# Kernel tuning notes

Measured on AMD Instinct MI355X. Metric: run time of the kernel, lower is better.

The kernel has to match this reference:

```python
import jax, jax.numpy as jnp
import numpy as np

B, L, D = 2, 2048, 1024
H, E = 16, 64  # n_heads, per-head dim (E_q=E_k=E_v)
EPS = 1e-5


def _layernorm(x):
    # fresh nn.LayerNorm each forward: gamma=1, beta=0, eps=1e-5 (biased var)
    mu = jnp.mean(x, axis=-1, keepdims=True)
    var = jnp.mean(jnp.square(x - mu), axis=-1, keepdims=True)
    return (x - mu) * jax.lax.rsqrt(var + EPS)


def setup_inputs() -> dict:
    key = jax.random.key(0)
    ks = jax.random.split(key, 9)
    s_in = 1.0 / np.sqrt(D)
    s_ctx = 1.0 / np.sqrt(H * E)
    return {
        "query": jax.random.normal(ks[0], (B, L, D), jnp.float32),
        "key": jax.random.normal(ks[1], (B, L, D), jnp.float32),
        "value": jax.random.normal(ks[2], (B, L, D), jnp.float32),
        # torch nn.Linear weights are [out_features, in_features]
        "W_Q": jax.random.uniform(ks[3], (H * E, D), jnp.float32, -s_in, s_in),
        "W_K": jax.random.uniform(ks[4], (H * E, D), jnp.float32, -s_in, s_in),
        "W_V": jax.random.uniform(ks[5], (H * E, D), jnp.float32, -s_in, s_in),
        "W_O": jax.random.uniform(ks[6], (D, H * E), jnp.float32, -s_ctx, s_ctx),
        "fc_w": jax.random.uniform(ks[7], (D, D), jnp.float32, -s_in, s_in),
        "fc_b": jax.random.uniform(ks[8], (D,), jnp.float32, -s_in, s_in),
    }


def reference(query, key, value, W_Q, W_K, W_V, W_O, fc_w, fc_b):
    b = query.shape[0]
    # projections -> [B, H, L, E]
    q = (query @ W_Q.T).reshape(b, -1, H, E).transpose(0, 2, 1, 3)
    k = (key @ W_K.T).reshape(b, -1, H, E).transpose(0, 2, 1, 3)
    v = (value @ W_V.T).reshape(b, -1, H, E).transpose(0, 2, 1, 3)
    scores = jnp.einsum('bhqe,bhke->bhqk', q, k) / np.sqrt(E).astype(np.float32)
    A = jax.nn.softmax(scores, axis=-1)                 # [B,H,Lq,Lk]
    ctx = jnp.einsum('bhqk,bhke->bhqe', A, v)           # [B,H,L,E]
    ctx = ctx.transpose(0, 2, 1, 3).reshape(b, -1, H * E)
    attn_out = ctx @ W_O.T                               # dropout = identity (eval)
    x = _layernorm(attn_out + query)
    out = x @ fc_w.T + fc_b                              # dropout = identity (eval)
    out = _layernorm(x + out)
    return out
```

## Files before the change

### kernel.cpp

```cpp
#include <hip/hip_runtime.h>
#include <stdint.h>

typedef unsigned short u16;
typedef __bf16 bf16x8 __attribute__((ext_vector_type(8)));
typedef __bf16 bf16x4 __attribute__((ext_vector_type(4)));
typedef short s16x4 __attribute__((ext_vector_type(4)));
typedef float f32x4 __attribute__((ext_vector_type(4)));

#define MFMA16(a,b,c) __builtin_amdgcn_mfma_f32_16x16x32_bf16((a),(b),(c),0,0,0)

__device__ __forceinline__ f32x4 mfma_k16(bf16x4 a, bf16x4 b, f32x4 c){
#if __has_builtin(__builtin_amdgcn_mfma_f32_16x16x16_bf16)
  return __builtin_amdgcn_mfma_f32_16x16x16_bf16(a, b, c, 0, 0, 0);
#elif __has_builtin(__builtin_amdgcn_mfma_f32_16x16x16bf16_1k)
  s16x4 ai, bi;
  __builtin_memcpy(&ai, &a, 8);
  __builtin_memcpy(&bi, &b, 8);
  return __builtin_amdgcn_mfma_f32_16x16x16bf16_1k(ai, bi, c, 0, 0, 0);
#else
  asm("v_mfma_f32_16x16x16_bf16 %0, %1, %2, %0" : "+v"(c) : "v"(a), "v"(b));
  return c;
#endif
}

__device__ __forceinline__ bf16x4 pack4(float a, float b, float c, float d){
  bf16x4 r; r[0]=(__bf16)a; r[1]=(__bf16)b; r[2]=(__bf16)c; r[3]=(__bf16)d; return r;
}

__device__ __forceinline__ void gl2lds16(const void* g, void* l){
  __builtin_amdgcn_global_load_lds(
      (const __attribute__((address_space(1))) unsigned int*)g,
      (__attribute__((address_space(3))) unsigned int*)l, 16, 0, 0);
}

__device__ __forceinline__ bf16x8 ldsfrag(const u16* base, int row, int gr){
  return *(const bf16x8*)(base + row * 64 + ((gr ^ (row & 7)) << 3));
}
__device__ __forceinline__ bf16x4 ldsfrag64(const u16* base, int row, int gr, int h){
  return *(const bf16x4*)(base + row * 64 + ((gr ^ (row & 7)) << 3) + (h << 2));
}

template<int NB, int BN>
__device__ __forceinline__ void gemm_core(const u16* __restrict__ A,
                                          const u16* __restrict__ Bt,
                                          int N, int K, int mode,
                                          void* __restrict__ Cout,
                                          const float* __restrict__ bias,
                                          float oscale)
{
  constexpr int NF = BN / 32;
  __shared__ u16 Al[NB][128 * 64];
  __shared__ u16 Bl[NB][BN * 64];
  const int tid  = threadIdx.x;
  const int lane = tid & 63;
  const int w    = tid >> 6;
  const int wr   = w >> 1, wc = w & 1;
  const int l15  = lane & 15, g = lane >> 4;
  const int rowBase = blockIdx.y << 7;
  const int colBase = blockIdx.x * BN;

  const int srow = tid >> 3;
  const int swz  = ((tid & 7) ^ (srow & 7)) << 3;
  const u16* Ag = A  + (size_t)(rowBase + srow) * K + swz;
  const u16* Bg = Bt + (size_t)(colBase + srow) * K + swz;

  f32x4 acc[4][NF];
#pragma unroll
  for (int m = 0; m < 4; ++m)
#pragma unroll
    for (int n = 0; n < NF; ++n) acc[m][n] = f32x4{0.f, 0.f, 0.f, 0.f};

  auto stage = [&](int buf, int k0) {
#pragma unroll
    for (int i = 0; i < 4; ++i)
      gl2lds16(Ag + (size_t)(i * 32) * K + k0, Al[buf] + i * 2048 + w * 512);
#pragma unroll
    for (int i = 0; i < BN / 32; ++i)
      gl2lds16(Bg + (size_t)(i * 32) * K + k0, Bl[buf] + i * 2048 + w * 512);
  };
  auto compute = [&](int buf) {
    __builtin_amdgcn_s_setprio(1);
#pragma unroll
    for (int kk = 0; kk < 2; ++kk) {
      bf16x8 af[4], bfr[NF];
#pragma unroll
      for (int m = 0; m < 4; ++m) af[m]  = ldsfrag(Al[buf], wr * 64 + m * 16 + l15, kk * 4 + g);
#pragma unroll
      for (int n = 0; n < NF; ++n) bfr[n] = ldsfrag(Bl[buf], wc * (BN/2) + n * 16 + l15, kk * 4 + g);
#pragma unroll
      for (int m = 0; m < 4; ++m)
#pragma unroll
        for (int n = 0; n < NF; ++n)
          acc[m][n] = MFMA16(af[m], bfr[n], acc[m][n]);
    }
    __builtin_amdgcn_s_setprio(0);
  };

  if (NB == 2) {
    stage(0, 0);
    __syncthreads();
    int cur = 0;
    for (int k0 = 0; k0 < K; k0 += 64) {
      if (k0 + 64 < K) stage(cur ^ 1, k0 + 64);
      compute(cur);
      __syncthreads();
      cur ^= 1;
    }
  } else {
    for (int k0 = 0; k0 < K; k0 += 64) {
      stage(0, k0);
      __syncthreads();
      compute(0);
      __syncthreads();
    }
  }

#pragma unroll
  for (int m = 0; m < 4; ++m) {
#pragma unroll
    for (int n = 0; n < NF; ++n) {
      const int row0 = rowBase + wr * 64 + m * 16 + g * 4;
      const int col  = colBase + wc * (BN/2) + n * 16 + l15;
      if (mode == 1) {
        const int b = row0 >> 11, l = row0 & 2047;
        const int h = col >> 6,  e = col & 63;
        *(bf16x4*)((u16*)Cout + ((size_t)((((b << 4) + h) << 6) | e) << 11) + l) =
            pack4(acc[m][n][0], acc[m][n][1], acc[m][n][2], acc[m][n][3]);
      } else {
        const float bb = (mode == 4) ? bias[col] : 0.f;
#pragma unroll
        for (int r = 0; r < 4; ++r) {
          const int row = row0 + r;
          const float v = acc[m][n][r];
          if (mode == 0) {
            *(__bf16*)((u16*)Cout + (size_t)row * N + col) = (__bf16)(v * oscale);
          } else {
            *(__bf16*)((u16*)Cout + (size_t)row * N + col) = (__bf16)(v + bb);
          }
        }
      }
    }
  }
}

#define QSCALE 0.18033688011112042f

__global__ __launch_bounds__(256) void k_proj(
    const u16* __restrict__ qb, const u16* __restrict__ kb, const u16* __restrict__ vb,
    const u16* __restrict__ wq, const u16* __restrict__ wk, const u16* __restrict__ wv,
    u16* __restrict__ Qp, u16* __restrict__ Kp, u16* __restrict__ Vt)
{
  const int z = blockIdx.z;
  const u16* A = (z == 0) ? qb : (z == 1) ? kb : vb;
  const u16* B = (z == 0) ? wq : (z == 1) ? wk : wv;
  void* C = (z == 0) ? (void*)Qp : (z == 1) ? (void*)Kp : (void*)Vt;
  gemm_core<2, 64>(A, B, 1024, 1024, (z == 2) ? 1 : 0, C, nullptr, (z == 0) ? QSCALE : 1.0f);
}

__global__ __launch_bounds__(256) void k_gemm_o(const u16* __restrict__ A,
                                                const u16* __restrict__ B,
                                                u16* __restrict__ C)
{ gemm_core<2, 64>(A, B, 1024, 1024, 0, (void*)C, nullptr, 1.0f); }

__global__ __launch_bounds__(256) void k_gemm_fc(const u16* __restrict__ A,
                                                 const u16* __restrict__ B,
                                                 u16* __restrict__ C,
                                                 const float* __restrict__ bias)
{ gemm_core<2, 64>(A, B, 1024, 1024, 4, (void*)C, bias, 1.0f); }

__global__ __launch_bounds__(256, 4) void k_attn(const u16* __restrict__ Qp,
                                                 const u16* __restrict__ Kp,
                                                 const u16* __restrict__ Vt,
                                                 float* __restrict__ Opart,
                                                 float* __restrict__ dpart)
{
  __shared__ u16 Klds[2][64 * 64];
  __shared__ u16 Vlds[2][64 * 64];

  const int tid = threadIdx.x, lane = tid & 63, w = tid >> 6;
  const int l15 = lane & 15, g = lane >> 4;
  const int bh = blockIdx.y, b = bh >> 4, h = bh & 15;
  const int q0 = blockIdx.x << 7;
  const int half = blockIdx.z;
  const int kvbase = half << 10;

  bf16x8 bq[2][2];
#pragma unroll
  for (int u = 0; u < 2; ++u) {
    const u16* Qr = Qp + (((size_t)((b << 11) + q0 + (w << 5) + (u << 4) + l15)) << 10)
                  + (h << 6) + (g << 3);
    bq[u][0] = *(const bf16x8*)(Qr);
    bq[u][1] = *(const bf16x8*)(Qr + 32);
  }

  const f32x4 zero4 = {0.f, 0.f, 0.f, 0.f};
  f32x4 o0[4], o1[4];
#pragma unroll
  for (int f = 0; f < 4; ++f) { o0[f] = zero4; o1[f] = zero4; }
  float ds0 = 0.f, ds1 = 0.f;

  const int srow = tid >> 3;
  const int swz  = ((tid & 7) ^ (srow & 7)) << 3;
  const u16* Kg = Kp + (((size_t)((b << 11) + kvbase + srow)) << 10) + (h << 6) + swz;
  const u16* Vg = Vt + (((size_t)((bh << 6) + srow)) << 11) + kvbase + swz;

  auto stage = [&](int buf, int j0) {
#pragma unroll
    for (int i = 0; i < 2; ++i) {
      gl2lds16(Kg + ((size_t)(j0 + i * 32) << 10), Klds[buf] + i * 2048 + w * 512);
      gl2lds16(Vg + ((size_t)(i * 32) << 11) + j0, Vlds[buf] + i * 2048 + w * 512);
    }
  };

  stage(0, 0);
  __syncthreads();
  int cur = 0;

  for (int j0 = 0; j0 < 1024; j0 += 64) {
    if (j0 + 64 < 1024) stage(cur ^ 1, j0 + 64);

    f32x4 s0[4], s1[4];
    __builtin_amdgcn_s_setprio(1);
#pragma unroll
    for (int f = 0; f < 4; ++f) {
      const bf16x8 ka = ldsfrag(Klds[cur], f * 16 + l15, g);
      const bf16x8 kb = ldsfrag(Klds[cur], f * 16 + l15, 4 + g);
      s0[f] = MFMA16(ka, bq[0][0], zero4);
      s0[f] = MFMA16(kb, bq[0][1], s0[f]);
      s1[f] = MFMA16(ka, bq[1][0], zero4);
      s1[f] = MFMA16(kb, bq[1][1], s1[f]);
    }
    __builtin_amdgcn_s_setprio(0);

    bf16x4 p0[4], p1[4];
#pragma unroll
    for (int f = 0; f < 4; ++f) {
      const float a0 = __builtin_amdgcn_exp2f(s0[f][0]);
      const float a1 = __builtin_amdgcn_exp2f(s0[f][1]);
      const float a2 = __builtin_amdgcn_exp2f(s0[f][2]);
      const float a3 = __builtin_amdgcn_exp2f(s0[f][3]);
      ds0 += (a0 + a1) + (a2 + a3);
      p0[f] = pack4(a0, a1, a2, a3);
      const float c0 = __builtin_amdgcn_exp2f(s1[f][0]);
      const float c1 = __builtin_amdgcn_exp2f(s1[f][1]);
      const float c2 = __builtin_amdgcn_exp2f(s1[f][2]);
      const float c3 = __builtin_amdgcn_exp2f(s1[f][3]);
      ds1 += (c0 + c1) + (c2 + c3);
      p1[f] = pack4(c0, c1, c2, c3);
    }

    __builtin_amdgcn_s_setprio(1);
#pragma unroll
    for (int fe = 0; fe < 4; ++fe) {
#pragma unroll
      for (int f = 0; f < 4; ++f) {
        const bf16x4 va = ldsfrag64(Vlds[cur], fe * 16 + l15, 2 * f + (g >> 1), g & 1);
        o0[fe] = mfma_k16(va, p0[f], o0[fe]);
        o1[fe] = mfma_k16(va, p1[f], o1[fe]);
      }
    }
    __builtin_amdgcn_s_setprio(0);
    __syncthreads();
    cur ^= 1;
  }

  ds0 += __shfl_xor(ds0, 16, 64);
  ds0 += __shfl_xor(ds0, 32, 64);
  ds1 += __shfl_xor(ds1, 16, 64);
  ds1 += __shfl_xor(ds1, 32, 64);

  const int brow0 = (b << 11) + q0 + (w << 5) + l15;
  const int brow1 = brow0 + 16;
  float* Op = Opart + ((size_t)half << 22);
#pragma unroll
  for (int f = 0; f < 4; ++f) {
    *(f32x4*)(Op + ((size_t)brow0 << 10) + (h << 6) + f * 16 + (g << 2)) = o0[f];
    *(f32x4*)(Op + ((size_t)brow1 << 10) + (h << 6) + f * 16 + (g << 2)) = o1[f];
  }
  if (g == 0) {
    dpart[(half << 16) + (brow0 << 4) + h] = ds0;
    dpart[(half << 16) + (brow1 << 4) + h] = ds1;
  }
}

__global__ __launch_bounds__(256) void k_combine(const float* __restrict__ Opart,
                                                 const float* __restrict__ dpart,
                                                 u16* __restrict__ ctx)
{
  const int row = blockIdx.x, tid = threadIdx.x;
  const int h = tid >> 4;
  const float d = dpart[(row << 4) + h] + dpart[(1 << 16) + (row << 4) + h];
  const float inv = 1.0f / d;
  const f32x4 p0 = ((const f32x4*)(Opart + ((size_t)row << 10)))[tid];
  const f32x4 p1 = ((const f32x4*)(Opart + (1u << 22) + ((size_t)row << 10)))[tid];
  ((bf16x4*)(ctx + ((size_t)row << 10)))[tid] =
      pack4((p0[0] + p1[0]) * inv, (p0[1] + p1[1]) * inv,
            (p0[2] + p1[2]) * inv, (p0[3] + p1[3]) * inv);
}

__device__ __forceinline__ void ln_stats(float4 t, int tid, float& mean, float& inv){
  float s = t.x + t.y + t.z + t.w;
  float q = t.x * t.x + t.y * t.y + t.z * t.z + t.w * t.w;
#pragma unroll
  for (int d = 1; d < 64; d <<= 1) {
    s += __shfl_xor(s, d, 64);
    q += __shfl_xor(q, d, 64);
  }
  __shared__ float ps[4], pq[4];
  const int w = tid >> 6;
  if ((tid & 63) == 0) { ps[w] = s; pq[w] = q; }
  __syncthreads();
  s = ps[0] + ps[1] + ps[2] + ps[3];
  q = pq[0] + pq[1] + pq[2] + pq[3];
  mean = s * (1.0f / 1024.0f);
  const float var = q * (1.0f / 1024.0f) - mean * mean;
  inv = rsqrtf(var + 1e-5f);
}

__global__ __launch_bounds__(256) void k_ln1(const u16* __restrict__ a,
                                             const float* __restrict__ res,
                                             u16* __restrict__ xb)
{
  const int row = blockIdx.x, tid = threadIdx.x;
  const size_t base = (size_t)row << 10;
  const bf16x4 av = ((const bf16x4*)(a + base))[tid];
  const float4 rr = ((const float4*)(res + base))[tid];
  float4 t;
  t.x = (float)av[0] + rr.x; t.y = (float)av[1] + rr.y;
  t.z = (float)av[2] + rr.z; t.w = (float)av[3] + rr.w;
  float mean, inv;
  ln_stats(t, tid, mean, inv);
  ((bf16x4*)(xb + base))[tid] = pack4((t.x - mean) * inv, (t.y - mean) * inv,
                                      (t.z - mean) * inv, (t.w - mean) * inv);
}

__global__ __launch_bounds__(256) void k_ln2(const u16* __restrict__ a,
                                             const u16* __restrict__ res,
                                             float* __restrict__ out)
{
  const int row = blockIdx.x, tid = threadIdx.x;
  const size_t base = (size_t)row << 10;
  const bf16x4 av = ((const bf16x4*)(a + base))[tid];
  const bf16x4 rv = ((const bf16x4*)(res + base))[tid];
  float4 t;
  t.x = (float)av[0] + (float)rv[0]; t.y = (float)av[1] + (float)rv[1];
  t.z = (float)av[2] + (float)rv[2]; t.w = (float)av[3] + (float)rv[3];
  float mean, inv;
  ln_stats(t, tid, mean, inv);
  float4 o;
  o.x = (t.x - mean) * inv; o.y = (t.y - mean) * inv;
  o.z = (t.z - mean) * inv; o.w = (t.w - mean) * inv;
  ((float4*)(out + base))[tid] = o;
}

__global__ __launch_bounds__(256) void k_cvt3(const float* __restrict__ q,
                                              const float* __restrict__ k,
                                              const float* __restrict__ v,
                                              u16* __restrict__ qo,
                                              u16* __restrict__ ko,
                                              u16* __restrict__ vo)
{
  const int z = blockIdx.y;
  const float* src = (z == 0) ? q : (z == 1) ? k : v;
  u16* dst = (z == 0) ? qo : (z == 1) ? ko : vo;
  const int i = blockIdx.x * 256 + threadIdx.x;
  const float4 t = ((const float4*)src)[i];
  ((bf16x4*)dst)[i] = pack4(t.x, t.y, t.z, t.w);
}

__global__ __launch_bounds__(256) void k_cvt5(const float* __restrict__ a0,
                                              const float* __restrict__ a1,
                                              const float* __restrict__ a2,
                                              const float* __restrict__ a3,
                                              const float* __restrict__ a4,
                                              u16* __restrict__ o0, u16* __restrict__ o1,
                                              u16* __restrict__ o2, u16* __restrict__ o3,
                                              u16* __restrict__ o4)
{
  const int z = blockIdx.y;
  const float* src = (z == 0) ? a0 : (z == 1) ? a1 : (z == 2) ? a2 : (z == 3) ? a3 : a4;
  u16* dst = (z == 0) ? o0 : (z == 1) ? o1 : (z == 2) ? o2 : (z == 3) ? o3 : o4;
  const int i = blockIdx.x * 256 + threadIdx.x;
  const float4 t = ((const float4*)src)[i];
  ((bf16x4*)dst)[i] = pack4(t.x, t.y, t.z, t.w);
}

extern "C" void kernel_launch(void* const* d_in, const int* in_sizes, int n_in,
                              void* d_out, int out_size, void* d_ws, size_t ws_size,
                              hipStream_t stream)
{
  (void)in_sizes; (void)n_in; (void)out_size; (void)ws_size;
  const float* query = (const float*)d_in[0];
  const float* key   = (const float*)d_in[1];
  const float* value = (const float*)d_in[2];
  const float* W_Q   = (const float*)d_in[3];
  const float* W_K   = (const float*)d_in[4];
  const float* W_V   = (const float*)d_in[5];
  const float* W_O   = (const float*)d_in[6];
  const float* fc_w  = (const float*)d_in[7];
  const float* fc_b  = (const float*)d_in[8];
  float* out = (float*)d_out;
  char* ws = (char*)d_ws;

  u16*   qb    = (u16*)(ws + 0);
  u16*   kb    = (u16*)(ws + 8388608);
  u16*   vb    = (u16*)(ws + 16777216);
  u16*   wq    = (u16*)(ws + 25165824);
  u16*   wk    = (u16*)(ws + 27262976);
  u16*   wv    = (u16*)(ws + 29360128);
  u16*   wo    = (u16*)(ws + 31457280);
  u16*   fw    = (u16*)(ws + 33554432);
  u16*   Qp    = (u16*)(ws + 35651584);
  u16*   Kp    = (u16*)(ws + 44040192);
  u16*   Vt    = (u16*)(ws + 52428800);
  u16*   ctx   = (u16*)(ws + 60817408);
  float* Opart = (float*)(ws + 69206016);
  float* dpart = (float*)(ws + 102760448);
  u16*   attnb = (u16*)(ws + 69206016);
  u16*   xb    = vb;
  u16*   yb    = qb;

  k_cvt3<<<dim3(4096, 3), 256, 0, stream>>>(query, key, value, qb, kb, vb);
  k_cvt5<<<dim3(1024, 5), 256, 0, stream>>>(W_Q, W_K, W_V, W_O, fc_w, wq, wk, wv, wo, fw);
  k_proj<<<dim3(16, 32, 3), 256, 0, stream>>>(qb, kb, vb, wq, wk, wv, Qp, Kp, Vt);
  k_attn<<<dim3(16, 32, 2), 256, 0, stream>>>(Qp, Kp, Vt, Opart, dpart);
  k_combine<<<dim3(4096), 256, 0, stream>>>(Opart, dpart, ctx);
  k_gemm_o<<<dim3(16, 32), 256, 0, stream>>>(ctx, wo, attnb);
  k_ln1<<<dim3(4096), 256, 0, stream>>>(attnb, query, xb);
  k_gemm_fc<<<dim3(16, 32), 256, 0, stream>>>(xb, fw, yb, fc_b);
  k_ln2<<<dim3(4096), 256, 0, stream>>>(yb, xb, out);
}
```

Measured before the change: 159.1 us.

## Fuse fp32-to-bf16 input conversion into projection GEMM and store attention partials as bf16

The projection GEMM now reads the fp32 query/key/value activations directly. It converts them to bf16 in registers and writes them into LDS, software-pipelined across the K loop, which removes the separate k_cvt3 kernel and its bf16 round-trip through memory. The split-KV attention partial outputs are also stored as bf16 instead of fp32, which halves the write and read traffic of the combine step. In exchange the A operand loses its async global-to-LDS path and needs extra registers, and rounding the unnormalized partials to bf16 adds a small amount of error.

```diff
diff --git a/kernel.cpp b/kernel.cpp
--- a/kernel.cpp
+++ b/kernel.cpp
@@ -26,6 +26,12 @@
 __device__ __forceinline__ bf16x4 pack4(float a, float b, float c, float d){
   bf16x4 r; r[0]=(__bf16)a; r[1]=(__bf16)b; r[2]=(__bf16)c; r[3]=(__bf16)d; return r;
 }
+__device__ __forceinline__ bf16x8 pack8(float4 a, float4 b){
+  bf16x8 r;
+  r[0]=(__bf16)a.x; r[1]=(__bf16)a.y; r[2]=(__bf16)a.z; r[3]=(__bf16)a.w;
+  r[4]=(__bf16)b.x; r[5]=(__bf16)b.y; r[6]=(__bf16)b.z; r[7]=(__bf16)b.w;
+  return r;
+}
 
 __device__ __forceinline__ void gl2lds16(const void* g, void* l){
   __builtin_amdgcn_global_load_lds(
@@ -40,8 +46,8 @@
   return *(const bf16x4*)(base + row * 64 + ((gr ^ (row & 7)) << 3) + (h << 2));
 }
 
-template<int NB, int BN>
-__device__ __forceinline__ void gemm_core(const u16* __restrict__ A,
+template<int BN, bool AF32>
+__device__ __forceinline__ void gemm_core(const void* __restrict__ Araw,
                                           const u16* __restrict__ Bt,
                                           int N, int K, int mode,
                                           void* __restrict__ Cout,
@@ -49,8 +55,8 @@
                                           float oscale)
 {
   constexpr int NF = BN / 32;
-  __shared__ u16 Al[NB][128 * 64];
-  __shared__ u16 Bl[NB][BN * 64];
+  __shared__ u16 Al[2][128 * 64];
+  __shared__ u16 Bl[2][BN * 64];
   const int tid  = threadIdx.x;
   const int lane = tid & 63;
   const int w    = tid >> 6;
@@ -61,8 +67,9 @@
 
   const int srow = tid >> 3;
   const int swz  = ((tid & 7) ^ (srow & 7)) << 3;
-  const u16* Ag = A  + (size_t)(rowBase + srow) * K + swz;
-  const u16* Bg = Bt + (size_t)(colBase + srow) * K + swz;
+  const u16*   Ag  = AF32 ? nullptr : (const u16*)Araw + (size_t)(rowBase + srow) * K + swz;
+  const float* Agf = AF32 ? (const float*)Araw + (size_t)(rowBase + srow) * K + swz : nullptr;
+  const u16*   Bg  = Bt + (size_t)(colBase + srow) * K + swz;
 
   f32x4 acc[4][NF];
 #pragma unroll
@@ -70,10 +77,28 @@
 #pragma unroll
     for (int n = 0; n < NF; ++n) acc[m][n] = f32x4{0.f, 0.f, 0.f, 0.f};
 
-  auto stage = [&](int buf, int k0) {
+  float4 ar[4][2];
+  auto loadA = [&](int k0) {
+    if (AF32) {
+#pragma unroll
+      for (int i = 0; i < 4; ++i) {
+        const float* p = Agf + (size_t)(i * 32) * K + k0;
+        ar[i][0] = *(const float4*)p;
+        ar[i][1] = *(const float4*)(p + 4);
+      }
+    }
+  };
+  auto writeA = [&](int buf) {
+#pragma unroll
+    for (int i = 0; i < 4; ++i)
+      *(bf16x8*)(Al[buf] + i * 2048 + tid * 8) = pack8(ar[i][0], ar[i][1]);
+  };
+  auto stageA = [&](int buf, int k0) {
 #pragma unroll
     for (int i = 0; i < 4; ++i)
       gl2lds16(Ag + (size_t)(i * 32) * K + k0, Al[buf] + i * 2048 + w * 512);
+  };
+  auto stageB = [&](int buf, int k0) {
 #pragma unroll
     for (int i = 0; i < BN / 32; ++i)
       gl2lds16(Bg + (size_t)(i * 32) * K + k0, Bl[buf] + i * 2048 + w * 512);
@@ -96,23 +121,21 @@
     __builtin_amdgcn_s_setprio(0);
   };
 
-  if (NB == 2) {
-    stage(0, 0);
+  if (AF32) { loadA(0); stageB(0, 0); writeA(0); }
+  else      { stageA(0, 0); stageB(0, 0); }
+  __syncthreads();
+  int cur = 0;
+  for (int k0 = 0; k0 < K; k0 += 64) {
+    const bool more = (k0 + 64) < K;
+    if (more) {
+      if (AF32) loadA(k0 + 64);
+      else      stageA(cur ^ 1, k0 + 64);
+      stageB(cur ^ 1, k0 + 64);
+    }
+    compute(cur);
+    if (more && AF32) writeA(cur ^ 1);
     __syncthreads();
-    int cur = 0;
-    for (int k0 = 0; k0 < K; k0 += 64) {
-      if (k0 + 64 < K) stage(cur ^ 1, k0 + 64);
-      compute(cur);
-      __syncthreads();
-      cur ^= 1;
-    }
-  } else {
-    for (int k0 = 0; k0 < K; k0 += 64) {
-      stage(0, k0);
-      __syncthreads();
-      compute(0);
-      __syncthreads();
-    }
+    cur ^= 1;
   }
 
 #pragma unroll
@@ -146,32 +169,32 @@
 #define QSCALE 0.18033688011112042f
 
 __global__ __launch_bounds__(256) void k_proj(
-    const u16* __restrict__ qb, const u16* __restrict__ kb, const u16* __restrict__ vb,
+    const float* __restrict__ qf, const float* __restrict__ kf, const float* __restrict__ vf,
     const u16* __restrict__ wq, const u16* __restrict__ wk, const u16* __restrict__ wv,
     u16* __restrict__ Qp, u16* __restrict__ Kp, u16* __restrict__ Vt)
 {
   const int z = blockIdx.z;
-  const u16* A = (z == 0) ? qb : (z == 1) ? kb : vb;
+  const float* A = (z == 0) ? qf : (z == 1) ? kf : vf;
   const u16* B = (z == 0) ? wq : (z == 1) ? wk : wv;
   void* C = (z == 0) ? (void*)Qp : (z == 1) ? (void*)Kp : (void*)Vt;
-  gemm_core<2, 64>(A, B, 1024, 1024, (z == 2) ? 1 : 0, C, nullptr, (z == 0) ? QSCALE : 1.0f);
+  gemm_core<64, true>(A, B, 1024, 1024, (z == 2) ? 1 : 0, C, nullptr, (z == 0) ? QSCALE : 1.0f);
 }
 
 __global__ __launch_bounds__(256) void k_gemm_o(const u16* __restrict__ A,
                                                 const u16* __restrict__ B,
                                                 u16* __restrict__ C)
-{ gemm_core<2, 64>(A, B, 1024, 1024, 0, (void*)C, nullptr, 1.0f); }
+{ gemm_core<64, false>(A, B, 1024, 1024, 0, (void*)C, nullptr, 1.0f); }
 
 __global__ __launch_bounds__(256) void k_gemm_fc(const u16* __restrict__ A,
                                                  const u16* __restrict__ B,
                                                  u16* __restrict__ C,
                                                  const float* __restrict__ bias)
-{ gemm_core<2, 64>(A, B, 1024, 1024, 4, (void*)C, bias, 1.0f); }
+{ gemm_core<64, false>(A, B, 1024, 1024, 4, (void*)C, bias, 1.0f); }
 
 __global__ __launch_bounds__(256, 4) void k_attn(const u16* __restrict__ Qp,
                                                  const u16* __restrict__ Kp,
                                                  const u16* __restrict__ Vt,
-                                                 float* __restrict__ Opart,
+                                                 u16* __restrict__ Opart,
                                                  float* __restrict__ dpart)
 {
   __shared__ u16 Klds[2][64 * 64];
@@ -271,11 +294,13 @@
 
   const int brow0 = (b << 11) + q0 + (w << 5) + l15;
   const int brow1 = brow0 + 16;
-  float* Op = Opart + ((size_t)half << 22);
+  u16* Op = Opart + ((size_t)half << 22);
 #pragma unroll
   for (int f = 0; f < 4; ++f) {
-    *(f32x4*)(Op + ((size_t)brow0 << 10) + (h << 6) + f * 16 + (g << 2)) = o0[f];
-    *(f32x4*)(Op + ((size_t)brow1 << 10) + (h << 6) + f * 16 + (g << 2)) = o1[f];
+    *(bf16x4*)(Op + (((size_t)brow0) << 10) + (h << 6) + f * 16 + (g << 2)) =
+        pack4(o0[f][0], o0[f][1], o0[f][2], o0[f][3]);
+    *(bf16x4*)(Op + (((size_t)brow1) << 10) + (h << 6) + f * 16 + (g << 2)) =
+        pack4(o1[f][0], o1[f][1], o1[f][2], o1[f][3]);
   }
   if (g == 0) {
     dpart[(half << 16) + (brow0 << 4) + h] = ds0;
@@ -283,7 +308,7 @@
   }
 }
 
-__global__ __launch_bounds__(256) void k_combine(const float* __restrict__ Opart,
+__global__ __launch_bounds__(256) void k_combine(const u16* __restrict__ Opart,
                                                  const float* __restrict__ dpart,
                                                  u16* __restrict__ ctx)
 {
@@ -291,11 +316,11 @@
   const int h = tid >> 4;
   const float d = dpart[(row << 4) + h] + dpart[(1 << 16) + (row << 4) + h];
   const float inv = 1.0f / d;
-  const f32x4 p0 = ((const f32x4*)(Opart + ((size_t)row << 10)))[tid];
-  const f32x4 p1 = ((const f32x4*)(Opart + (1u << 22) + ((size_t)row << 10)))[tid];
+  const bf16x4 p0 = ((const bf16x4*)(Opart + ((size_t)row << 10)))[tid];
+  const bf16x4 p1 = ((const bf16x4*)(Opart + (1u << 22) + ((size_t)row << 10)))[tid];
   ((bf16x4*)(ctx + ((size_t)row << 10)))[tid] =
-      pack4((p0[0] + p1[0]) * inv, (p0[1] + p1[1]) * inv,
-            (p0[2] + p1[2]) * inv, (p0[3] + p1[3]) * inv);
+      pack4(((float)p0[0] + (float)p1[0]) * inv, ((float)p0[1] + (float)p1[1]) * inv,
+            ((float)p0[2] + (float)p1[2]) * inv, ((float)p0[3] + (float)p1[3]) * inv);
 }
 
 __device__ __forceinline__ void ln_stats(float4 t, int tid, float& mean, float& inv){
@@ -353,21 +378,6 @@
   ((float4*)(out + base))[tid] = o;
 }
 
-__global__ __launch_bounds__(256) void k_cvt3(const float* __restrict__ q,
-                                              const float* __restrict__ k,
-                                              const float* __restrict__ v,
-                                              u16* __restrict__ qo,
-                                              u16* __restrict__ ko,
-                                              u16* __restrict__ vo)
-{
-  const int z = blockIdx.y;
-  const float* src = (z == 0) ? q : (z == 1) ? k : v;
-  u16* dst = (z == 0) ? qo : (z == 1) ? ko : vo;
-  const int i = blockIdx.x * 256 + threadIdx.x;
-  const float4 t = ((const float4*)src)[i];
-  ((bf16x4*)dst)[i] = pack4(t.x, t.y, t.z, t.w);
-}
-
 __global__ __launch_bounds__(256) void k_cvt5(const float* __restrict__ a0,
                                               const float* __restrict__ a1,
                                               const float* __restrict__ a2,
@@ -402,9 +412,8 @@
   float* out = (float*)d_out;
   char* ws = (char*)d_ws;
 
-  u16*   qb    = (u16*)(ws + 0);
-  u16*   kb    = (u16*)(ws + 8388608);
-  u16*   vb    = (u16*)(ws + 16777216);
+  u16*   xb    = (u16*)(ws + 0);
+  u16*   yb    = (u16*)(ws + 8388608);
   u16*   wq    = (u16*)(ws + 25165824);
   u16*   wk    = (u16*)(ws + 27262976);
   u16*   wv    = (u16*)(ws + 29360128);
@@ -414,15 +423,12 @@
   u16*   Kp    = (u16*)(ws + 44040192);
   u16*   Vt    = (u16*)(ws + 52428800);
   u16*   ctx   = (u16*)(ws + 60817408);
-  float* Opart = (float*)(ws + 69206016);
-  float* dpart = (float*)(ws + 102760448);
+  u16*   Opart = (u16*)(ws + 69206016);
+  float* dpart = (float*)(ws + 85983232);
   u16*   attnb = (u16*)(ws + 69206016);
-  u16*   xb    = vb;
-  u16*   yb    = qb;
-
-  k_cvt3<<<dim3(4096, 3), 256, 0, stream>>>(query, key, value, qb, kb, vb);
+
   k_cvt5<<<dim3(1024, 5), 256, 0, stream>>>(W_Q, W_K, W_V, W_O, fc_w, wq, wk, wv, wo, fw);
-  k_proj<<<dim3(16, 32, 3), 256, 0, stream>>>(qb, kb, vb, wq, wk, wv, Qp, Kp, Vt);
+  k_proj<<<dim3(16, 32, 3), 256, 0, stream>>>(query, key, value, wq, wk, wv, Qp, Kp, Vt);
   k_attn<<<dim3(16, 32, 2), 256, 0, stream>>>(Qp, Kp, Vt, Opart, dpart);
   k_combine<<<dim3(4096), 256, 0, stream>>>(Opart, dpart, ctx);
   k_gemm_o<<<dim3(16, 32), 256, 0, stream>>>(ctx, wo, attnb);
```

New measurement: 176.7 us. +11.0%, slower.
